# Kernel optimization log

Hardware: AMD Instinct MI355X
Metric: run time of the kernel (lower is better)

Reference implementation:

```python
import jax, jax.numpy as jnp
import numpy as np

IN_DIM = 128
MEM_DIM = 256
NUM_CLASSES = 12
NUM_LEVELS = 17  # complete binary tree, N = 2**17 - 1 = 131071 nodes


def setup_inputs() -> dict:
    key = jax.random.key(0)
    ks = jax.random.split(key, 7)
    N = 2 ** NUM_LEVELS - 1
    s = 1.0 / np.sqrt(MEM_DIM)  # PyTorch LSTMCell/Linear init scale
    return {
        "x": jax.random.normal(ks[0], (N, IN_DIM), dtype=jnp.float32),
        "W_ih": jax.random.uniform(ks[1], (4 * MEM_DIM, IN_DIM), jnp.float32, -s, s),
        "b_ih": jax.random.uniform(ks[2], (4 * MEM_DIM,), jnp.float32, -s, s),
        "W_hh": jax.random.uniform(ks[3], (4 * MEM_DIM, MEM_DIM), jnp.float32, -s, s),
        "b_hh": jax.random.uniform(ks[4], (4 * MEM_DIM,), jnp.float32, -s, s),
        "W_fc": jax.random.uniform(ks[5], (NUM_CLASSES, MEM_DIM), jnp.float32, -s, s),
        "b_fc": jax.random.uniform(ks[6], (NUM_CLASSES,), jnp.float32, -s, s),
        "num_levels": NUM_LEVELS,
    }


def reference(x, W_ih, b_ih, W_hh, b_hh, W_fc, b_fc, num_levels):
    # Complete binary tree in BFS order: level l occupies nodes [2^l-1, 2^(l+1)-2];
    # children of level-l nodes are exactly the (contiguous) level-(l+1) nodes.
    mem = W_hh.shape[1]
    h_below = None
    c_below = None
    for l in reversed(range(num_levels)):
        n = 2 ** l
        x_l = x[n - 1:2 * n - 1]  # [n, in_dim] nodes at this level
        if h_below is None:  # leaves: zero child state
            ch_h = jnp.zeros((n, mem), dtype=x.dtype)
            ch_c = ch_h
        else:  # sum the two children's (h, c), as the recursion accumulates
            ch_h = h_below.reshape(n, 2, mem).sum(axis=1)
            ch_c = c_below.reshape(n, 2, mem).sum(axis=1)
        # PyTorch LSTMCell: gates = x W_ih^T + b_ih + h W_hh^T + b_hh, chunks i,f,g,o
        gates = x_l @ W_ih.T + b_ih + ch_h @ W_hh.T + b_hh  # [n, 4*mem]
        i, f, g, o = jnp.split(gates, 4, axis=-1)
        c_new = jax.nn.sigmoid(f) * ch_c + jax.nn.sigmoid(i) * jnp.tanh(g)
        h_new = jax.nn.sigmoid(o) * jnp.tanh(c_new)
        h_below, c_below = h_new, c_new
    # Original applies FC to state[1] == cell state c of the root (kept faithfully).
    return c_below[:1] @ W_fc.T + b_fc  # [1, num_classes]
```

## Files before the change

kernel.cpp:

```cpp
#include <hip/hip_runtime.h>
#include <hip/hip_bf16.h>
#include <cstddef>

#define IN_DIM 128
#define MEM 256
#define KTOT 384
#define NLEAF 65536
#define NBLK_TAIL 8

typedef float f32x4 __attribute__((ext_vector_type(4)));
typedef short s16x8 __attribute__((ext_vector_type(8)));
typedef unsigned int u32;

__device__ inline unsigned short f2bf(float f){
    unsigned int u = __builtin_bit_cast(unsigned int, f);
    u += 0x7fff + ((u >> 16) & 1);
    return (unsigned short)(u >> 16);
}

__device__ inline void gld_lds16(const void* g, void* l){
    __builtin_amdgcn_global_load_lds((const __attribute__((address_space(1))) u32*)g,
                                     (__attribute__((address_space(3))) u32*)l, 16, 0, 0);
}

__device__ inline float fsigm(float x){
    return __builtin_amdgcn_rcpf(1.f + __expf(-x));
}
__device__ inline float ftanh(float x){
    return 2.f * __builtin_amdgcn_rcpf(1.f + __expf(-2.f * x)) - 1.f;
}

__host__ __device__ inline size_t offA(int l){
    if (l == 16) return 0;
    return 8388608u + 384u * (65536u - (1u << (l + 1)));
}
#define ARENA_ELEMS 33554048u
#define ARENA_PAD   65536u

__device__ inline void grid_barrier(unsigned* ctr, unsigned target){
    __syncthreads();
    if (threadIdx.x == 0){
        __threadfence();
        __hip_atomic_fetch_add(ctr, 1u, __ATOMIC_RELEASE, __HIP_MEMORY_SCOPE_AGENT);
        while (__hip_atomic_load(ctr, __ATOMIC_RELAXED, __HIP_MEMORY_SCOPE_AGENT) < target)
            __builtin_amdgcn_s_sleep(2);
    }
    __syncthreads();
    __threadfence();
}

__global__ void pack_kernel(const float* __restrict__ x,
                            const float* __restrict__ W_ih, const float* __restrict__ b_ih,
                            const float* __restrict__ W_hh, const float* __restrict__ b_hh,
                            unsigned short* __restrict__ Wp, float* __restrict__ bp,
                            unsigned short* __restrict__ Aarena, unsigned* __restrict__ ctr){
    const int stride = gridDim.x * blockDim.x;
    const int tid0 = blockIdx.x * blockDim.x + threadIdx.x;
    if (tid0 == 0){ ctr[0] = 0; }

    for (int g = tid0; g < 1024 * 48; g += stride){
        int row = g / 48, ko = (g - row * 48) * 8;
        const float* s = (ko < IN_DIM) ? (W_ih + (size_t)row * IN_DIM + ko)
                                       : (W_hh + (size_t)row * MEM + (ko - IN_DIM));
        f32x4 v0 = *(const f32x4*)s, v1 = *(const f32x4*)(s + 4);
        s16x8 o;
        #pragma unroll
        for (int e = 0; e < 4; ++e){ o[e] = (short)f2bf(v0[e]); o[4+e] = (short)f2bf(v1[e]); }
        *(s16x8*)(Wp + (size_t)row * KTOT + ko) = o;
        if (ko == 0) bp[row] = b_ih[row] + b_hh[row];
    }

    const int TOTAL_G = 131071 * 16;
    for (int g = tid0; g < TOTAL_G; g += stride){
        int i  = g >> 4;
        int ko = (g & 15) * 8;
        int l  = 31 - __clz(i + 1);
        int j  = i + 1 - (1 << l);
        size_t dst = offA(l) + (size_t)j * ((l == 16) ? 128 : 384) + ko;
        const f32x4* s = (const f32x4*)(x + (size_t)i * IN_DIM + ko);
        f32x4 v0 = s[0], v1 = s[1];
        s16x8 o;
        #pragma unroll
        for (int e = 0; e < 4; ++e){ o[e] = (short)f2bf(v0[e]); o[4+e] = (short)f2bf(v1[e]); }
        *(s16x8*)(Aarena + dst) = o;
    }
}

template<int NK>
__global__ __launch_bounds__(512, 1) void gemm_lstm8p_kernel(
    const unsigned short* __restrict__ A, int n,
    const unsigned short* __restrict__ Wp, const float* __restrict__ bp,
    const float* __restrict__ csum_in,
    unsigned short* __restrict__ A_next, float* __restrict__ csum_out)
{
    __shared__ __align__(16) unsigned short As[2][2][128 * 64];
    __shared__ __align__(16) unsigned short Bs[2][2][128 * 64];

    const int tid  = threadIdx.x;
    const int lane = tid & 63;
    const int wid  = tid >> 6;
    const int wm   = wid >> 2;
    const int wn   = wid & 3;
    const int row0 = blockIdx.x * 256;
    const int m0   = blockIdx.y * 64;
    const int mg   = m0 + wn * 16 + (lane & 15);

    auto stageA = [&](int kt, int h){
        #pragma unroll
        for (int i = 0; i < 2; ++i){
            int p  = i * 512 + tid;
            int r  = p >> 3;
            int ls = (p & 7) ^ (r & 7);
            gld_lds16(A + (size_t)(row0 + h * 128 + r) * NK + kt * 64 + ls * 8,
                      (char*)As[kt & 1][h] + (size_t)(i * 512 + wid * 64) * 16);
        }
    };
    auto stageB = [&](int kt, int h){
        #pragma unroll
        for (int i = 0; i < 2; ++i){
            int p  = i * 512 + tid;
            int r  = p >> 3;
            int b  = h * 128 + r;
            int grow = (b >> 6) * 256 + m0 + (b & 63);
            int ls = (p & 7) ^ (r & 7);
            gld_lds16(Wp + (size_t)grow * KTOT + kt * 64 + ls * 8,
                      (char*)Bs[kt & 1][h] + (size_t)(i * 512 + wid * 64) * 16);
        }
    };

    f32x4 acc[8][4];
    #pragma unroll
    for (int r = 0; r < 8; ++r)
        #pragma unroll
        for (int q = 0; q < 4; ++q)
            acc[r][q] = (f32x4){0.f, 0.f, 0.f, 0.f};

    constexpr int nkt = NK / 64;
    stageA(0, 0); stageA(0, 1); stageB(0, 0);
    if (nkt > 1) stageB(1, 0);
    stageB(0, 1);

    s16x8 bfr[2][2];

    #pragma unroll
    for (int t = 0; t < nkt; ++t){
        const unsigned short* Ab = As[t & 1][wm];
        const unsigned short* Bb0 = Bs[t & 1][0];
        const unsigned short* Bb1 = Bs[t & 1][1];

        if (t + 1 < nkt) { asm volatile("s_waitcnt vmcnt(4)" ::: "memory"); }
        else             { asm volatile("s_waitcnt vmcnt(2)" ::: "memory"); }
        __builtin_amdgcn_s_barrier();
        asm volatile("" ::: "memory");

        #pragma unroll
        for (int rh = 0; rh < 2; ++rh){
            s16x8 a[4][2];
            #pragma unroll
            for (int j = 0; j < 4; ++j)
                #pragma unroll
                for (int ks = 0; ks < 2; ++ks){
                    int kb = (((ks * 4 + (lane >> 4)) ^ (lane & 7))) * 8;
                    a[j][ks] = *(const s16x8*)(Ab + (size_t)(rh * 64 + j * 16 + (lane & 15)) * 64 + kb);
                }
            if (rh == 0){
                #pragma unroll
                for (int q2 = 0; q2 < 2; ++q2)
                    #pragma unroll
                    for (int ks = 0; ks < 2; ++ks){
                        int kb = (((ks * 4 + (lane >> 4)) ^ (lane & 7))) * 8;
                        bfr[q2][ks] = *(const s16x8*)(Bb0 + (size_t)(q2 * 64 + wn * 16 + (lane & 15)) * 64 + kb);
                    }
                if (t + 1 < nkt) stageA(t + 1, 0);
            } else {
                if (t + 1 < nkt) stageA(t + 1, 1);
            }
            __builtin_amdgcn_s_setprio(1);
            #pragma unroll
            for (int j = 0; j < 4; ++j)
                #pragma unroll
                for (int q2 = 0; q2 < 2; ++q2)
                    #pragma unroll
                    for (int ks = 0; ks < 2; ++ks)
                        acc[rh * 4 + j][q2] = __builtin_amdgcn_mfma_f32_16x16x32_bf16(
                            a[j][ks], bfr[q2][ks], acc[rh * 4 + j][q2], 0, 0, 0);
            __builtin_amdgcn_s_setprio(0);
        }

        if (t + 1 < nkt) { asm volatile("s_waitcnt vmcnt(4)" ::: "memory"); }
        else             { asm volatile("s_waitcnt vmcnt(0)" ::: "memory"); }
        __builtin_amdgcn_s_barrier();
        asm volatile("" ::: "memory");

        #pragma unroll
        for (int rh = 0; rh < 2; ++rh){
            s16x8 a[4][2];
            #pragma unroll
            for (int j = 0; j < 4; ++j)
                #pragma unroll
                for (int ks = 0; ks < 2; ++ks){
                    int kb = (((ks * 4 + (lane >> 4)) ^ (lane & 7))) * 8;
                    a[j][ks] = *(const s16x8*)(Ab + (size_t)(rh * 64 + j * 16 + (lane & 15)) * 64 + kb);
                }
            if (rh == 0){
                #pragma unroll
                for (int q2 = 0; q2 < 2; ++q2)
                    #pragma unroll
                    for (int ks = 0; ks < 2; ++ks){
                        int kb = (((ks * 4 + (lane >> 4)) ^ (lane & 7))) * 8;
                        bfr[q2][ks] = *(const s16x8*)(Bb1 + (size_t)(q2 * 64 + wn * 16 + (lane & 15)) * 64 + kb);
                    }
                if (t + 2 < nkt) stageB(t + 2, 0);
            } else {
                if (t + 1 < nkt) stageB(t + 1, 1);
            }
            __builtin_amdgcn_s_setprio(1);
            #pragma unroll
            for (int j = 0; j < 4; ++j)
                #pragma unroll
                for (int q2 = 0; q2 < 2; ++q2)
                    #pragma unroll
                    for (int ks = 0; ks < 2; ++ks)
                        acc[rh * 4 + j][2 + q2] = __builtin_amdgcn_mfma_f32_16x16x32_bf16(
                            a[j][ks], bfr[q2][ks], acc[rh * 4 + j][2 + q2], 0, 0, 0);
            __builtin_amdgcn_s_setprio(0);
        }
        __builtin_amdgcn_s_barrier();
        asm volatile("" ::: "memory");
    }

    const float b0 = bp[0 * 256 + mg];
    const float b1 = bp[1 * 256 + mg];
    const float b2 = bp[2 * 256 + mg];
    const float b3 = bp[3 * 256 + mg];
    #pragma unroll
    for (int r = 0; r < 8; ++r){
        const int base = row0 + wm * 128 + r * 16 + (lane >> 4) * 4;
        float cpre[4];
        #pragma unroll
        for (int e = 0; e < 4; ++e)
            cpre[e] = csum_in[(size_t)(base + e) * MEM + mg];
        float cn[4], hn[4];
        #pragma unroll
        for (int e = 0; e < 4; ++e){
            float iv = acc[r][0][e] + b0;
            float fv = acc[r][1][e] + b1;
            float gv = acc[r][2][e] + b2;
            float ov = acc[r][3][e] + b3;
            float c  = fsigm(fv) * cpre[e] + fsigm(iv) * ftanh(gv);
            cn[e] = c;
            hn[e] = fsigm(ov) * ftanh(c);
        }
        int p0 = base >> 1;
        A_next[(size_t)p0 * KTOT + IN_DIM + mg] = f2bf(hn[0] + hn[1]);
        csum_out[(size_t)p0 * MEM + mg] = cn[0] + cn[1];
        A_next[(size_t)(p0 + 1) * KTOT + IN_DIM + mg] = f2bf(hn[2] + hn[3]);
        csum_out[(size_t)(p0 + 1) * MEM + mg] = cn[2] + cn[3];
    }
}

#define BM 128
#define KC 64

template<int NK>
__global__ __launch_bounds__(256) void gemm_lstm_kernel(
    const unsigned short* __restrict__ A, int n,
    const unsigned short* __restrict__ Wp, const float* __restrict__ bp,
    const float* __restrict__ csum_in, int leaf,
    unsigned short* __restrict__ A_next, float* __restrict__ csum_out)
{
    __shared__ __align__(16) unsigned short As[2][BM * KC];
    __shared__ __align__(16) unsigned short Bs[2][BM * KC];

    const int tid  = threadIdx.x;
    const int lane = tid & 63;
    const int wid  = tid >> 6;
    const int wm   = wid >> 1;
    const int wc   = wid & 1;
    const int row0 = blockIdx.x * BM;
    const int m0   = blockIdx.y * 32;

    const int srow = lane >> 3;
    const int scol = ((lane & 7) ^ srow) * 8;

    const int mg = m0 + wc * 16 + (lane & 15);

    const float b0 = bp[0 * 256 + mg];
    const float b1 = bp[1 * 256 + mg];
    const float b2 = bp[2 * 256 + mg];
    const float b3 = bp[3 * 256 + mg];
    float cpre[4][4];
    if (!leaf){
        #pragma unroll
        for (int r = 0; r < 4; ++r){
            const int base = row0 + wm * 64 + r * 16 + (lane >> 4) * 4;
            #pragma unroll
            for (int e = 0; e < 4; ++e)
                cpre[r][e] = csum_in[(size_t)(base + e) * MEM + mg];
        }
    } else {
        #pragma unroll
        for (int r = 0; r < 4; ++r)
            #pragma unroll
            for (int e = 0; e < 4; ++e) cpre[r][e] = 0.f;
    }

    f32x4 acc[4][4];
    #pragma unroll
    for (int r = 0; r < 4; ++r)
        #pragma unroll
        for (int q = 0; q < 4; ++q)
            acc[r][q] = (f32x4){0.f, 0.f, 0.f, 0.f};

    auto stage = [&](int d, int kk){
        char* asb = (char*)As[d];
        char* bsb = (char*)Bs[d];
        #pragma unroll
        for (int q = 0; q < 4; ++q){
            int t = wid * 4 + q;
            int r = t * 8 + srow;
            gld_lds16(A + (size_t)(row0 + r) * NK + kk + scol, asb + t * 1024);
        }
        #pragma unroll
        for (int q = 0; q < 4; ++q){
            int t = wid * 4 + q;
            int b = t * 8 + srow;
            int grow = (b >> 5) * 256 + m0 + (b & 31);
            gld_lds16(Wp + (size_t)grow * KTOT + kk + scol, bsb + t * 1024);
        }
    };

    constexpr int nIter = NK / KC;
    stage(0, 0);
    int buf = 0;
    #pragma unroll
    for (int it = 0; it < nIter; ++it){
        if (it + 1 < nIter){
            stage(buf ^ 1, (it + 1) * KC);
            asm volatile("s_waitcnt vmcnt(8)" ::: "memory");
        } else {
            asm volatile("s_waitcnt vmcnt(0)" ::: "memory");
        }
        __builtin_amdgcn_s_barrier();
        const unsigned short* Ab = As[buf];
        const unsigned short* Bb = Bs[buf];
        #pragma unroll
        for (int ks = 0; ks < 2; ++ks){
            const int slot = ks * 4 + (lane >> 4);
            const int kb = (slot ^ (lane & 7)) * 8;
            s16x8 a[4], b[4];
            #pragma unroll
            for (int r = 0; r < 4; ++r)
                a[r] = *(const s16x8*)(Ab + (wm * 64 + r * 16 + (lane & 15)) * KC + kb);
            #pragma unroll
            for (int q = 0; q < 4; ++q)
                b[q] = *(const s16x8*)(Bb + (q * 32 + wc * 16 + (lane & 15)) * KC + kb);
            #pragma unroll
            for (int r = 0; r < 4; ++r)
                #pragma unroll
                for (int q = 0; q < 4; ++q)
                    acc[r][q] = __builtin_amdgcn_mfma_f32_16x16x32_bf16(a[r], b[q], acc[r][q], 0, 0, 0);
        }
        __builtin_amdgcn_s_barrier();
        buf ^= 1;
    }

    #pragma unroll
    for (int r = 0; r < 4; ++r){
        const int base = row0 + wm * 64 + r * 16 + (lane >> 4) * 4;
        float cn[4], hn[4];
        #pragma unroll
        for (int e = 0; e < 4; ++e){
            float iv = acc[r][0][e] + b0;
            float fv = acc[r][1][e] + b1;
            float gv = acc[r][2][e] + b2;
            float ov = acc[r][3][e] + b3;
            float c  = fsigm(fv) * cpre[r][e] + fsigm(iv) * ftanh(gv);
            cn[e] = c;
            hn[e] = fsigm(ov) * ftanh(c);
        }
        if (base < n){
            int p0 = base >> 1;
            A_next[(size_t)p0 * KTOT + IN_DIM + mg] = f2bf(hn[0] + hn[1]);
            csum_out[(size_t)p0 * MEM + mg] = cn[0] + cn[1];
        }
        if (base + 2 < n){
            int p1 = (base >> 1) + 1;
            A_next[(size_t)p1 * KTOT + IN_DIM + mg] = f2bf(hn[2] + hn[3]);
            csum_out[(size_t)p1 * MEM + mg] = cn[2] + cn[3];
        }
    }
}

__global__ __launch_bounds__(256) void tail_kernel(
    const unsigned short* __restrict__ arena,
    const unsigned short* __restrict__ Wp, const float* __restrict__ bp,
    float* cs_in, float* cs_out,
    float* __restrict__ c_root,
    const float* __restrict__ W_fc, const float* __restrict__ b_fc,
    float* __restrict__ out, unsigned* __restrict__ ctr)
{
    __shared__ __align__(16) unsigned short WpL[128 * KTOT];
    __shared__ __align__(16) unsigned short AL[64 * KTOT];

    const int tid  = threadIdx.x;
    const int lane = tid & 63;
    const int wid  = tid >> 6;
    const int wm   = wid >> 1;
    const int wc   = wid & 1;
    const int m0   = blockIdx.x * 32;
    const int mg   = m0 + wc * 16 + (lane & 15);

    #pragma unroll
    for (int i = 0; i < 24; ++i){
        int p0 = wid * 1536 + i * 64;
        int p  = p0 + lane;
        int lrow  = p / 48;
        int pslot = p % 48;
        int lslot = pslot ^ (lrow & 7);
        int grow  = (lrow >> 5) * 256 + m0 + (lrow & 31);
        gld_lds16(Wp + (size_t)grow * KTOT + lslot * 8, (char*)WpL + (size_t)p0 * 16);
    }

    const float b0 = bp[0 * 256 + mg];
    const float b1 = bp[1 * 256 + mg];
    const float b2 = bp[2 * 256 + mg];
    const float b3 = bp[3 * 256 + mg];

    asm volatile("s_waitcnt vmcnt(0)" ::: "memory");
    __builtin_amdgcn_s_barrier();

    unsigned gen = 0;
    for (int l = 7; l >= 0; --l){
        const int n = 1 << l;
        const unsigned short* Al = arena + offA(l);
        const int nhalf = (n > 64) ? (n >> 6) : 1;

        for (int h = 0; h < nhalf; ++h){
            const int r0 = h * 64;
            const int rows = (n < 64) ? n : 64;

            const int nslots = rows * 48;
            for (int t = 0; t * 256 < nslots; ++t){
                int pbase = t * 256 + wid * 64;
                int p = pbase + lane;
                if (p < nslots){
                    int row   = p / 48;
                    int pslot = p - row * 48;
                    int lslot = pslot ^ (row & 7);
                    gld_lds16(Al + (size_t)(r0 + row) * KTOT + lslot * 8,
                              (char*)AL + (size_t)pbase * 16);
                }
            }

            float cpre[2][4];
            #pragma unroll
            for (int r = 0; r < 2; ++r){
                const int base = r0 + wm * 32 + r * 16 + (lane >> 4) * 4;
                #pragma unroll
                for (int e = 0; e < 4; ++e)
                    cpre[r][e] = cs_in[(size_t)(base + e) * MEM + mg];
            }

            asm volatile("s_waitcnt vmcnt(0)" ::: "memory");
            __builtin_amdgcn_s_barrier();

            f32x4 acc[2][4];
            #pragma unroll
            for (int r = 0; r < 2; ++r)
                #pragma unroll
                for (int q = 0; q < 4; ++q)
                    acc[r][q] = (f32x4){0.f, 0.f, 0.f, 0.f};

            #pragma unroll
            for (int kc = 0; kc < 12; ++kc){
                const int ls = kc * 4 + (lane >> 4);
                const int kb = (ls ^ (lane & 7)) * 8;
                s16x8 a[2], b[4];
                #pragma unroll
                for (int r = 0; r < 2; ++r)
                    a[r] = *(const s16x8*)(AL + (size_t)(wm * 32 + r * 16 + (lane & 15)) * KTOT + kb);
                #pragma unroll
                for (int q = 0; q < 4; ++q)
                    b[q] = *(const s16x8*)(WpL + (q * 32 + wc * 16 + (lane & 15)) * KTOT + kb);
                #pragma unroll
                for (int r = 0; r < 2; ++r)
                    #pragma unroll
                    for (int q = 0; q < 4; ++q)
                        acc[r][q] = __builtin_amdgcn_mfma_f32_16x16x32_bf16(a[r], b[q], acc[r][q], 0, 0, 0);
            }

            #pragma unroll
            for (int r = 0; r < 2; ++r){
                const int base = r0 + wm * 32 + r * 16 + (lane >> 4) * 4;
                float cn[4], hn[4];
                #pragma unroll
                for (int e = 0; e < 4; ++e){
                    float iv = acc[r][0][e] + b0;
                    float fv = acc[r][1][e] + b1;
                    float gv = acc[r][2][e] + b2;
                    float ov = acc[r][3][e] + b3;
                    float c  = fsigm(fv) * cpre[r][e] + fsigm(iv) * ftanh(gv);
                    cn[e] = c;
                    hn[e] = fsigm(ov) * ftanh(c);
                }
                if (l == 0){
                    if (base == 0) c_root[mg] = cn[0];
                } else {
                    unsigned short* A_next = (unsigned short*)arena + offA(l - 1);
                    if (base < n){
                        int p0 = base >> 1;
                        A_next[(size_t)p0 * KTOT + IN_DIM + mg] = f2bf(hn[0] + hn[1]);
                        cs_out[(size_t)p0 * MEM + mg] = cn[0] + cn[1];
                    }
                    if (base + 2 < n){
                        int p1 = (base >> 1) + 1;
                        A_next[(size_t)p1 * KTOT + IN_DIM + mg] = f2bf(hn[2] + hn[3]);
                        cs_out[(size_t)p1 * MEM + mg] = cn[2] + cn[3];
                    }
                }
            }
            __builtin_amdgcn_s_barrier();
        }

        float* t = cs_in; cs_in = cs_out; cs_out = t;
        ++gen;
        grid_barrier(ctr, (unsigned)(NBLK_TAIL * gen));
    }

    if (blockIdx.x == 0){
        int w = wid;
        for (int cls = w * 3; cls < w * 3 + 3; ++cls){
            float s = 0.f;
            for (int m = lane; m < 256; m += 64)
                s += c_root[m] * W_fc[cls * 256 + m];
            #pragma unroll
            for (int off = 32; off; off >>= 1)
                s += __shfl_down(s, off, 64);
            if (lane == 0) out[cls] = s + b_fc[cls];
        }
    }
}

extern "C" void kernel_launch(void* const* d_in, const int* in_sizes, int n_in,
                              void* d_out, int out_size, void* d_ws, size_t ws_size,
                              hipStream_t stream)
{
    const float* x    = (const float*)d_in[0];
    const float* W_ih = (const float*)d_in[1];
    const float* b_ih = (const float*)d_in[2];
    const float* W_hh = (const float*)d_in[3];
    const float* b_hh = (const float*)d_in[4];
    const float* W_fc = (const float*)d_in[5];
    const float* b_fc = (const float*)d_in[6];
    float* out = (float*)d_out;

    const size_t OFF_WP = 0;
    const size_t OFF_BP = 786432;
    const size_t OFF_A  = 790528;
    const size_t OFF_CS0 = OFF_A + (size_t)(ARENA_ELEMS + ARENA_PAD) * 2;
    const size_t OFF_CS1 = OFF_CS0 + 33554432;
    const size_t OFF_CR  = OFF_CS1 + 33554432;
    const size_t OFF_CTR = OFF_CR + 1024;
    const size_t NEEDED  = OFF_CTR + 64;
    if (ws_size < NEEDED) return;

    char* ws = (char*)d_ws;
    unsigned short* Wp    = (unsigned short*)(ws + OFF_WP);
    float* bp             = (float*)(ws + OFF_BP);
    unsigned short* arena = (unsigned short*)(ws + OFF_A);
    float* cs0            = (float*)(ws + OFF_CS0);
    float* cs1            = (float*)(ws + OFF_CS1);
    float* c_root         = (float*)(ws + OFF_CR);
    unsigned* ctr         = (unsigned*)(ws + OFF_CTR);

    pack_kernel<<<dim3(2048), dim3(256), 0, stream>>>(
        x, W_ih, b_ih, W_hh, b_hh, Wp, bp, arena, ctr);

    gemm_lstm_kernel<IN_DIM><<<dim3(NLEAF / BM, 8), dim3(256), 0, stream>>>(
        arena + offA(16), NLEAF, Wp, bp,
        nullptr, 1, arena + offA(15), cs0);

    gemm_lstm8p_kernel<KTOT><<<dim3(128, 4), dim3(512), 0, stream>>>(
        arena + offA(15), 32768, Wp, bp, cs0, arena + offA(14), cs1);
    gemm_lstm8p_kernel<KTOT><<<dim3(64, 4), dim3(512), 0, stream>>>(
        arena + offA(14), 16384, Wp, bp, cs1, arena + offA(13), cs0);

    float* cs_in = cs0; float* cs_out = cs1;
    for (int l = 13; l >= 8; --l){
        int n = 1 << l;
        gemm_lstm_kernel<KTOT><<<dim3(n / BM, 8), dim3(256), 0, stream>>>(
            arena + offA(l), n, Wp, bp,
            cs_in, 0, arena + offA(l - 1), cs_out);
        float* t = cs_in; cs_in = cs_out; cs_out = t;
    }

    tail_kernel<<<dim3(NBLK_TAIL), dim3(256), 0, stream>>>(
        arena, Wp, bp, cs_in, cs_out, c_root, W_fc, b_fc, out, ctr);
}
```

Before: 213.0 us.

## Store child cell-state sums in fp16 and run leaf level on 8-wave kernel

The intermediate cell-state sum buffers move from fp32 to _Float16, halving their write and read traffic between levels and shrinking the workspace. The leaf level now uses the larger 512-thread gemm_lstm8p kernel with a leaf flag that zeroes the child cell state. Storing cell sums in fp16 loses precision across 17 levels of recurrence and may risk overflow if values grow. The leaf launch uses the NK=128 instantiation of the 8-wave kernel, whose staging must handle the shorter K.

```diff
diff --git a/kernel.cpp b/kernel.cpp
--- a/kernel.cpp
+++ b/kernel.cpp
@@ -90,8 +90,8 @@
 __global__ __launch_bounds__(512, 1) void gemm_lstm8p_kernel(
     const unsigned short* __restrict__ A, int n,
     const unsigned short* __restrict__ Wp, const float* __restrict__ bp,
-    const float* __restrict__ csum_in,
-    unsigned short* __restrict__ A_next, float* __restrict__ csum_out)
+    const _Float16* __restrict__ csum_in, int leaf,
+    unsigned short* __restrict__ A_next, _Float16* __restrict__ csum_out)
 {
     __shared__ __align__(16) unsigned short As[2][2][128 * 64];
     __shared__ __align__(16) unsigned short Bs[2][2][128 * 64];
@@ -239,7 +239,7 @@
         float cpre[4];
         #pragma unroll
         for (int e = 0; e < 4; ++e)
-            cpre[e] = csum_in[(size_t)(base + e) * MEM + mg];
+            cpre[e] = leaf ? 0.f : (float)csum_in[(size_t)(base + e) * MEM + mg];
         float cn[4], hn[4];
         #pragma unroll
         for (int e = 0; e < 4; ++e){
@@ -253,9 +253,9 @@
         }
         int p0 = base >> 1;
         A_next[(size_t)p0 * KTOT + IN_DIM + mg] = f2bf(hn[0] + hn[1]);
-        csum_out[(size_t)p0 * MEM + mg] = cn[0] + cn[1];
+        csum_out[(size_t)p0 * MEM + mg] = (_Float16)(cn[0] + cn[1]);
         A_next[(size_t)(p0 + 1) * KTOT + IN_DIM + mg] = f2bf(hn[2] + hn[3]);
-        csum_out[(size_t)(p0 + 1) * MEM + mg] = cn[2] + cn[3];
+        csum_out[(size_t)(p0 + 1) * MEM + mg] = (_Float16)(cn[2] + cn[3]);
     }
 }
 
@@ -266,8 +266,8 @@
 __global__ __launch_bounds__(256) void gemm_lstm_kernel(
     const unsigned short* __restrict__ A, int n,
     const unsigned short* __restrict__ Wp, const float* __restrict__ bp,
-    const float* __restrict__ csum_in, int leaf,
-    unsigned short* __restrict__ A_next, float* __restrict__ csum_out)
+    const _Float16* __restrict__ csum_in, int leaf,
+    unsigned short* __restrict__ A_next, _Float16* __restrict__ csum_out)
 {
     __shared__ __align__(16) unsigned short As[2][BM * KC];
     __shared__ __align__(16) unsigned short Bs[2][BM * KC];
@@ -296,7 +296,7 @@
             const int base = row0 + wm * 64 + r * 16 + (lane >> 4) * 4;
             #pragma unroll
             for (int e = 0; e < 4; ++e)
-                cpre[r][e] = csum_in[(size_t)(base + e) * MEM + mg];
+                cpre[r][e] = (float)csum_in[(size_t)(base + e) * MEM + mg];
         }
     } else {
         #pragma unroll
@@ -382,12 +382,12 @@
         if (base < n){
             int p0 = base >> 1;
             A_next[(size_t)p0 * KTOT + IN_DIM + mg] = f2bf(hn[0] + hn[1]);
-            csum_out[(size_t)p0 * MEM + mg] = cn[0] + cn[1];
+            csum_out[(size_t)p0 * MEM + mg] = (_Float16)(cn[0] + cn[1]);
         }
         if (base + 2 < n){
             int p1 = (base >> 1) + 1;
             A_next[(size_t)p1 * KTOT + IN_DIM + mg] = f2bf(hn[2] + hn[3]);
-            csum_out[(size_t)p1 * MEM + mg] = cn[2] + cn[3];
+            csum_out[(size_t)p1 * MEM + mg] = (_Float16)(cn[2] + cn[3]);
         }
     }
 }
@@ -395,7 +395,7 @@
 __global__ __launch_bounds__(256) void tail_kernel(
     const unsigned short* __restrict__ arena,
     const unsigned short* __restrict__ Wp, const float* __restrict__ bp,
-    float* cs_in, float* cs_out,
+    _Float16* cs_in, _Float16* cs_out,
     float* __restrict__ c_root,
     const float* __restrict__ W_fc, const float* __restrict__ b_fc,
     float* __restrict__ out, unsigned* __restrict__ ctr)
@@ -459,7 +459,7 @@
                 const int base = r0 + wm * 32 + r * 16 + (lane >> 4) * 4;
                 #pragma unroll
                 for (int e = 0; e < 4; ++e)
-                    cpre[r][e] = cs_in[(size_t)(base + e) * MEM + mg];
+                    cpre[r][e] = (float)cs_in[(size_t)(base + e) * MEM + mg];
             }
 
             asm volatile("s_waitcnt vmcnt(0)" ::: "memory");
@@ -511,19 +511,19 @@
                     if (base < n){
                         int p0 = base >> 1;
                         A_next[(size_t)p0 * KTOT + IN_DIM + mg] = f2bf(hn[0] + hn[1]);
-                        cs_out[(size_t)p0 * MEM + mg] = cn[0] + cn[1];
+                        cs_out[(size_t)p0 * MEM + mg] = (_Float16)(cn[0] + cn[1]);
                     }
                     if (base + 2 < n){
                         int p1 = (base >> 1) + 1;
                         A_next[(size_t)p1 * KTOT + IN_DIM + mg] = f2bf(hn[2] + hn[3]);
-                        cs_out[(size_t)p1 * MEM + mg] = cn[2] + cn[3];
+                        cs_out[(size_t)p1 * MEM + mg] = (_Float16)(cn[2] + cn[3]);
                     }
                 }
             }
             __builtin_amdgcn_s_barrier();
         }
 
-        float* t = cs_in; cs_in = cs_out; cs_out = t;
+        _Float16* t = cs_in; cs_in = cs_out; cs_out = t;
         ++gen;
         grid_barrier(ctr, (unsigned)(NBLK_TAIL * gen));
     }
@@ -559,8 +559,8 @@
     const size_t OFF_BP = 786432;
     const size_t OFF_A  = 790528;
     const size_t OFF_CS0 = OFF_A + (size_t)(ARENA_ELEMS + ARENA_PAD) * 2;
-    const size_t OFF_CS1 = OFF_CS0 + 33554432;
-    const size_t OFF_CR  = OFF_CS1 + 33554432;
+    const size_t OFF_CS1 = OFF_CS0 + 16777216;
+    const size_t OFF_CR  = OFF_CS1 + 16777216;
     const size_t OFF_CTR = OFF_CR + 1024;
     const size_t NEEDED  = OFF_CTR + 64;
     if (ws_size < NEEDED) return;
@@ -569,30 +569,30 @@
     unsigned short* Wp    = (unsigned short*)(ws + OFF_WP);
     float* bp             = (float*)(ws + OFF_BP);
     unsigned short* arena = (unsigned short*)(ws + OFF_A);
-    float* cs0            = (float*)(ws + OFF_CS0);
-    float* cs1            = (float*)(ws + OFF_CS1);
+    _Float16* cs0         = (_Float16*)(ws + OFF_CS0);
+    _Float16* cs1         = (_Float16*)(ws + OFF_CS1);
     float* c_root         = (float*)(ws + OFF_CR);
     unsigned* ctr         = (unsigned*)(ws + OFF_CTR);
 
     pack_kernel<<<dim3(2048), dim3(256), 0, stream>>>(
         x, W_ih, b_ih, W_hh, b_hh, Wp, bp, arena, ctr);
 
-    gemm_lstm_kernel<IN_DIM><<<dim3(NLEAF / BM, 8), dim3(256), 0, stream>>>(
+    gemm_lstm8p_kernel<IN_DIM><<<dim3(NLEAF / 256, 4), dim3(512), 0, stream>>>(
         arena + offA(16), NLEAF, Wp, bp,
         nullptr, 1, arena + offA(15), cs0);
 
     gemm_lstm8p_kernel<KTOT><<<dim3(128, 4), dim3(512), 0, stream>>>(
-        arena + offA(15), 32768, Wp, bp, cs0, arena + offA(14), cs1);
+        arena + offA(15), 32768, Wp, bp, cs0, 0, arena + offA(14), cs1);
     gemm_lstm8p_kernel<KTOT><<<dim3(64, 4), dim3(512), 0, stream>>>(
-        arena + offA(14), 16384, Wp, bp, cs1, arena + offA(13), cs0);
-
-    float* cs_in = cs0; float* cs_out = cs1;
+        arena + offA(14), 16384, Wp, bp, cs1, 0, arena + offA(13), cs0);
+
+    _Float16* cs_in = cs0; _Float16* cs_out = cs1;
     for (int l = 13; l >= 8; --l){
         int n = 1 << l;
         gemm_lstm_kernel<KTOT><<<dim3(n / BM, 8), dim3(256), 0, stream>>>(
             arena + offA(l), n, Wp, bp,
             cs_in, 0, arena + offA(l - 1), cs_out);
-        float* t = cs_in; cs_in = cs_out; cs_out = t;
+        _Float16* t = cs_in; cs_in = cs_out; cs_out = t;
     }
 
     tail_kernel<<<dim3(NBLK_TAIL), dim3(256), 0, stream>>>(
```

New measurement: 236.8 us. +11.2%, slower.
